# Kernel optimization log

Measured on AMD Instinct MI355X. Metric: run time of the kernel, lower is better.

Reference implementation:

```python
import jax, jax.numpy as jnp
import numpy as np

B, F, CTX, HID, L, NB = 16384, 64, 128, 512, 8, 2


def setup_inputs() -> dict:
    key = jax.random.key(0)
    ks = jax.random.split(key, 8)
    inputs = jax.random.normal(ks[0], (B, F), jnp.float32)
    context = jax.random.normal(ks[1], (B, CTX), jnp.float32)
    n_id = F // 2                      # identity features per coupling layer
    in_dim = n_id + CTX                # coupling net input = identity half + context
    out_dim = F                        # 2 * num_transform_features (shift | scale)
    s_in = 1.0 / np.sqrt(in_dim)
    s_h = 1.0 / np.sqrt(HID)
    W_in = jax.random.uniform(ks[2], (L, in_dim, HID), jnp.float32, -s_in, s_in)
    b_in = jax.random.uniform(ks[3], (L, HID), jnp.float32, -s_in, s_in)
    W_h = jax.random.uniform(ks[4], (L, NB, HID, HID), jnp.float32, -s_h, s_h)
    b_h = jax.random.uniform(ks[5], (L, NB, HID), jnp.float32, -s_h, s_h)
    # output layer init: normal(0, 0.01) weight, zero bias (as in torch source)
    W_out = 0.01 * jax.random.normal(ks[6], (L, HID, out_dim), jnp.float32)
    b_out = jnp.zeros((L, out_dim), jnp.float32)
    # fixed random permutations between coupling layers (nflows RandomPermutation buffers)
    rng = np.random.RandomState(42)
    perms = jnp.asarray(np.stack([rng.permutation(F) for _ in range(L - 1)]), jnp.int32)
    return dict(inputs=inputs, context=context, W_in=W_in, b_in=b_in,
                W_h=W_h, b_h=b_h, W_out=W_out, b_out=b_out, perms=perms)


def reference(inputs, context, W_in, b_in, W_h, b_h, W_out, b_out, perms):
    F_ = inputs.shape[-1]
    n_layers = W_in.shape[0]
    n_blocks = W_h.shape[1]
    nt = F_ // 2  # num transform features
    even_idx = jnp.arange(0, F_, 2)
    odd_idx = jnp.arange(1, F_, 2)
    x = jnp.clip(inputs, -1.0, 1.0)
    logdet = jnp.zeros(x.shape[0], x.dtype)
    for i in range(n_layers):
        # mask[::2]=1 for even layers -> mask>0 (even indices) are TRANSFORM features
        if i % 2 == 0:
            t_idx, id_idx = even_idx, odd_idx
        else:
            t_idx, id_idx = odd_idx, even_idx
        id_split = x[:, id_idx]   # [B, nt]
        tr_split = x[:, t_idx]    # [B, nt]
        h = jax.nn.relu(jnp.concatenate([id_split, context], -1) @ W_in[i] + b_in[i])
        for j in range(n_blocks):
            h = jax.nn.relu(h @ W_h[i, j] + b_h[i, j])
        p = h @ W_out[i] + b_out[i]            # [B, 2*nt]
        shift = p[:, :nt]
        scale = jax.nn.sigmoid(p[:, nt:] + 2.0) + 1e-3
        logdet = logdet + jnp.sum(jnp.log(scale), axis=-1)
        x = x.at[:, t_idx].set(tr_split * scale + shift).at[:, id_idx].set(id_split)
        if i < n_layers - 1:
            x = x[:, perms[i]]
    return jnp.clip(x, -1.0, 1.0), logdet
```

## Files before the change

kernel.cpp:

```cpp
#include <hip/hip_runtime.h>


typedef float v4f  __attribute__((ext_vector_type(4)));
typedef float v16f __attribute__((ext_vector_type(16)));
typedef int   v4i  __attribute__((ext_vector_type(4)));
typedef int   v8i  __attribute__((ext_vector_type(8)));
typedef unsigned char uchar;
typedef unsigned long long ull;

#define BATCH 16384
#define NF    64
#define NCTX  128
#define NL    8

#define RS     528
#define HHALF  256
#define AST    208
#define AHALF  96
#define PST    68

#define WSCALE     16.0f
#define WSCALE_INV 0.0625f

#define WIN_EPL   (192 * 512)
#define WH_EPB    (512 * 512)
#define WOUT_EPL  (512 * 64)
#define OFF_WIN   ((size_t)0)
#define OFF_WH    ((size_t)(8 * WIN_EPL))
#define OFF_WOUT  (OFF_WH + (size_t)(16 * WH_EPB))
#define TOT_PACK_ELEMS (OFF_WOUT + (size_t)(8 * WOUT_EPL))
#define NEED_WS   (TOT_PACK_ELEMS)

template<bool HI>
__device__ __forceinline__ unsigned int pk2(float a, float b, unsigned int old) {
    return __builtin_amdgcn_cvt_pk_fp8_f32(a, b, old, HI);
}
__device__ __forceinline__ uchar q8(float v) {
    return (uchar)(__builtin_amdgcn_cvt_pk_fp8_f32(v, v, 0u, false) & 0xffu);
}

__global__ void pack_weights_kernel(const float* __restrict__ W_in,
                                    const float* __restrict__ W_h,
                                    const float* __restrict__ W_out,
                                    unsigned char* __restrict__ ws) {
    const int TIN  = 8 * (WIN_EPL / 8);
    const int TH   = 16 * (WH_EPB / 8);
    const int TOUT = 8 * (WOUT_EPL / 8);
    int t = blockIdx.x * blockDim.x + threadIdx.x;
    if (t >= TIN + TH + TOUT) return;
    float v[8];
    if (t < TIN + TH) {
        const float* src; int r, rawK;
        if (t < TIN) {
            int i = t / (WIN_EPL / 8); r = t - i * (WIN_EPL / 8);
            src = W_in + (size_t)i * (160 * 512); rawK = 160;
        } else {
            int u = t - TIN; int ij = u >> 15; r = u & 32767;
            src = W_h + (size_t)ij * WH_EPB; rawK = 512;
        }
        int kb  = r >> 12, rem = r & 4095;
        int ls  = rem >> 2, g = rem & 3;
        int lane = ls & 63;
        int n = (ls >> 6) * 32 + (lane & 31);
        int pig = (g == 1) ? 2 : (g == 2) ? 1 : g;
        int k0 = kb * 64 + (lane >> 5) * 32 + pig * 8;
#pragma unroll
        for (int j = 0; j < 8; ++j) {
            int k = k0 + j;
            v[j] = (k < rawK) ? src[(size_t)k * 512 + n] * WSCALE : 0.f;
        }
    } else {
        int u = t - TIN - TH;
        int i = u >> 12, r = u & 4095;
        const float* src = W_out + (size_t)i * WOUT_EPL;
        int frag = r >> 6, lane = r & 63;
        int k0 = (frag >> 2) * 32 + (lane >> 4) * 8;
        int n  = (frag & 3) * 16 + (lane & 15);
#pragma unroll
        for (int j = 0; j < 8; ++j)
            v[j] = src[(size_t)(k0 + j) * 64 + n] * WSCALE;
    }
    uint2 o;
    o.x = pk2<false>(v[0], v[1], 0u);
    o.x = pk2<true >(v[2], v[3], o.x);
    o.y = pk2<false>(v[4], v[5], 0u);
    o.y = pk2<true >(v[6], v[7], o.y);
    *(uint2*)(ws + (size_t)t * 8) = o;
}

__device__ __forceinline__ v16f mfma32(ull a, ull b, v16f c) {
    return __builtin_amdgcn_mfma_f32_32x32x16_fp8_fp8((long)a, (long)b, c, 0, 0, 0);
}
__device__ __forceinline__ v4f mfma16(ull a, ull b, v4f c) {
    return __builtin_amdgcn_mfma_f32_16x16x32_fp8_fp8((long)a, (long)b, c, 0, 0, 0);
}
__device__ __forceinline__ v16f mfma64(v8i a, v8i b, v16f c) {
    return __builtin_amdgcn_mfma_scale_f32_32x32x64_f8f6f4(
        a, b, c, 0, 0, 0, 0x7f7f7f7f, 0, 0x7f7f7f7f);
}

template<int NKB>
__device__ __forceinline__ void gemm32mx(
    const uchar* __restrict__ wpk,
    const float* __restrict__ bias,
    const uchar* __restrict__ Abuf, int ast, int halfoff,
    uchar* __restrict__ Obuf,
    int strip, int lane)
{
    const int l31 = lane & 31, hl = lane >> 5;
    v16f acc0, acc1;
#pragma unroll
    for (int r = 0; r < 16; ++r) { acc0[r] = 0.f; acc1[r] = 0.f; }
    const uchar* aLo0 = Abuf + l31 * ast + hl * 16;
    const uchar* aHi0 = aLo0 + halfoff;
    const uchar* aLo1 = aLo0 + 32 * ast;
    const uchar* aHi1 = aHi0 + 32 * ast;
    const uchar* bptr = wpk + (size_t)(strip * 64 + lane) * 32;

    auto loadB = [&](int kb) -> v8i {
        if (kb >= NKB) kb = NKB - 1;
        const uchar* p = bptr + (size_t)kb * 32768;
        v4i lo = *(const v4i*)p;
        v4i hi = *(const v4i*)(p + 16);
        return __builtin_shufflevector(lo, hi, 0, 1, 2, 3, 4, 5, 6, 7);
    };
    auto loadA = [&](const uchar* lo_, const uchar* hi_, int kb) -> v8i {
        v4i lo = *(const v4i*)(lo_ + kb * 32);
        v4i hi = *(const v4i*)(hi_ + kb * 32);
        return __builtin_shufflevector(lo, hi, 0, 1, 2, 3, 4, 5, 6, 7);
    };

    v8i b0 = loadB(0), b1 = loadB(1), b2 = loadB(2), b3 = loadB(3);
#pragma unroll 1
    for (int kb = 0; kb + 3 < NKB; kb += 4) {
        acc0 = mfma64(loadA(aLo0, aHi0, kb + 0), b0, acc0);
        acc1 = mfma64(loadA(aLo1, aHi1, kb + 0), b0, acc1);
        b0 = loadB(kb + 4);
        acc0 = mfma64(loadA(aLo0, aHi0, kb + 1), b1, acc0);
        acc1 = mfma64(loadA(aLo1, aHi1, kb + 1), b1, acc1);
        b1 = loadB(kb + 5);
        acc0 = mfma64(loadA(aLo0, aHi0, kb + 2), b2, acc0);
        acc1 = mfma64(loadA(aLo1, aHi1, kb + 2), b2, acc1);
        b2 = loadB(kb + 6);
        acc0 = mfma64(loadA(aLo0, aHi0, kb + 3), b3, acc0);
        acc1 = mfma64(loadA(aLo1, aHi1, kb + 3), b3, acc1);
        b3 = loadB(kb + 7);
    }
    if constexpr ((NKB & 3) != 0) {
        constexpr int kb0 = NKB & ~3;
#pragma unroll
        for (int kb = kb0; kb < NKB; ++kb) {
            v8i bb = ((kb & 3) == 0) ? b0 : ((kb & 3) == 1) ? b1
                   : ((kb & 3) == 2) ? b2 : b3;
            acc0 = mfma64(loadA(aLo0, aHi0, kb), bb, acc0);
            acc1 = mfma64(loadA(aLo1, aHi1, kb), bb, acc1);
        }
    }

    const int n = strip * 32 + l31;
    const int nb = ((n >> 3) & 1) * HHALF + ((n >> 4) << 3) + (n & 7);
    const float bv = bias[n];
#pragma unroll
    for (int reg = 0; reg < 16; ++reg) {
        int row = (reg & 3) + 8 * (reg >> 2) + 4 * hl;
        float v0 = fmaxf(fmaf(acc0[reg], WSCALE_INV, bv), 0.f);
        Obuf[row * RS + nb] = q8(v0);
        float v1 = fmaxf(fmaf(acc1[reg], WSCALE_INV, bv), 0.f);
        Obuf[(row + 32) * RS + nb] = q8(v1);
    }
}

template<int KC>
__device__ __forceinline__ void gemm32_raw(
    const float* __restrict__ wraw,
    const float* __restrict__ bias,
    const uchar* __restrict__ Abuf, int ast, int ahalf,
    uchar* __restrict__ Obuf,
    int strip, int lane)
{
    constexpr int P = KC / 2;
    const int l31 = lane & 31, hl = lane >> 5;
    v16f acc0, acc1;
#pragma unroll
    for (int r = 0; r < 16; ++r) { acc0[r] = 0.f; acc1[r] = 0.f; }
    const uchar* a0p = Abuf + l31 * ast + hl * ahalf;
    const uchar* a1p = a0p + 32 * ast;

    auto loadB = [&](int kc) -> ull {
        if (kc >= KC) kc = KC - 1;
        int n  = strip * 32 + l31;
        int k0 = kc * 16 + hl * 8;
        unsigned int lo, hi;
        lo = pk2<false>(wraw[(size_t)(k0 + 0) * 512 + n] * WSCALE,
                        wraw[(size_t)(k0 + 1) * 512 + n] * WSCALE, 0u);
        lo = pk2<true >(wraw[(size_t)(k0 + 2) * 512 + n] * WSCALE,
                        wraw[(size_t)(k0 + 3) * 512 + n] * WSCALE, lo);
        hi = pk2<false>(wraw[(size_t)(k0 + 4) * 512 + n] * WSCALE,
                        wraw[(size_t)(k0 + 5) * 512 + n] * WSCALE, 0u);
        hi = pk2<true >(wraw[(size_t)(k0 + 6) * 512 + n] * WSCALE,
                        wraw[(size_t)(k0 + 7) * 512 + n] * WSCALE, hi);
        return ((ull)hi << 32) | (ull)lo;
    };

    ull b0 = loadB(0), b1 = loadB(1), b2 = loadB(2), b3 = loadB(3);
    int p2 = 0;
#pragma unroll 1
    for (; p2 + 1 < P; p2 += 2) {
        ulonglong2 Aa0 = *(const ulonglong2*)(a0p + p2 * 16);
        ulonglong2 Aa1 = *(const ulonglong2*)(a1p + p2 * 16);
        acc0 = mfma32(Aa0.x, b0, acc0);
        acc1 = mfma32(Aa1.x, b0, acc1);
        b0 = loadB(2 * p2 + 4);
        acc0 = mfma32(Aa0.y, b1, acc0);
        acc1 = mfma32(Aa1.y, b1, acc1);
        b1 = loadB(2 * p2 + 5);
        ulonglong2 Ab0 = *(const ulonglong2*)(a0p + p2 * 16 + 16);
        ulonglong2 Ab1 = *(const ulonglong2*)(a1p + p2 * 16 + 16);
        acc0 = mfma32(Ab0.x, b2, acc0);
        acc1 = mfma32(Ab1.x, b2, acc1);
        b2 = loadB(2 * p2 + 6);
        acc0 = mfma32(Ab0.y, b3, acc0);
        acc1 = mfma32(Ab1.y, b3, acc1);
        b3 = loadB(2 * p2 + 7);
    }
    if constexpr (P & 1) {
        ulonglong2 Aa0 = *(const ulonglong2*)(a0p + (P - 1) * 16);
        ulonglong2 Aa1 = *(const ulonglong2*)(a1p + (P - 1) * 16);
        acc0 = mfma32(Aa0.x, b0, acc0);
        acc1 = mfma32(Aa1.x, b0, acc1);
        acc0 = mfma32(Aa0.y, b1, acc0);
        acc1 = mfma32(Aa1.y, b1, acc1);
    }

    const int n = strip * 32 + l31;
    const int nb = ((n >> 3) & 1) * HHALF + ((n >> 4) << 3) + (n & 7);
    const float bv = bias[n];
#pragma unroll
    for (int reg = 0; reg < 16; ++reg) {
        int row = (reg & 3) + 8 * (reg >> 2) + 4 * hl;
        float v0 = fmaxf(fmaf(acc0[reg], WSCALE_INV, bv), 0.f);
        Obuf[row * RS + nb] = q8(v0);
        float v1 = fmaxf(fmaf(acc1[reg], WSCALE_INV, bv), 0.f);
        Obuf[(row + 32) * RS + nb] = q8(v1);
    }
}

template<bool PACKED>
__device__ __forceinline__ void gemm16_out(
    const uchar* __restrict__ wpk,
    const float* __restrict__ wraw,
    const float* __restrict__ bias,
    const uchar* __restrict__ Abuf,
    float* __restrict__ Pbuf,
    int mtb, int ntb, int lane)
{
    const int quad = lane >> 4, l15 = lane & 15;
    v4f acc; acc[0] = acc[1] = acc[2] = acc[3] = 0.f;
    const int row = mtb * 16 + l15;
    const uchar* ap = Abuf + row * RS + (quad & 1) * HHALF + ((quad >> 1) << 3);
    const uchar* bptr =
        PACKED ? wpk + (size_t)(ntb * 64 + lane) * 8 : (const uchar*)0;
    constexpr int KC = 16;

    auto loadB = [&](int kc) -> ull {
        if (kc >= KC) kc = KC - 1;
        if constexpr (PACKED) {
            return *(const ull*)(bptr + (size_t)kc * 2048);
        } else {
            int n  = ntb * 16 + l15;
            int k0 = kc * 32 + quad * 8;
            unsigned int lo, hi;
            lo = pk2<false>(wraw[(size_t)(k0 + 0) * 64 + n] * WSCALE,
                            wraw[(size_t)(k0 + 1) * 64 + n] * WSCALE, 0u);
            lo = pk2<true >(wraw[(size_t)(k0 + 2) * 64 + n] * WSCALE,
                            wraw[(size_t)(k0 + 3) * 64 + n] * WSCALE, lo);
            hi = pk2<false>(wraw[(size_t)(k0 + 4) * 64 + n] * WSCALE,
                            wraw[(size_t)(k0 + 5) * 64 + n] * WSCALE, 0u);
            hi = pk2<true >(wraw[(size_t)(k0 + 6) * 64 + n] * WSCALE,
                            wraw[(size_t)(k0 + 7) * 64 + n] * WSCALE, hi);
            return ((ull)hi << 32) | (ull)lo;
        }
    };
    auto step = [&](int kc, ull bb) {
        ull a = *(const ull*)(ap + kc * 16);
        acc = mfma16(a, bb, acc);
    };

    ull b0 = loadB(0), b1 = loadB(1), b2 = loadB(2), b3 = loadB(3);
    int kc = 0;
#pragma unroll 1
    for (; kc + 3 < KC; kc += 4) {
        step(kc + 0, b0); b0 = loadB(kc + 4);
        step(kc + 1, b1); b1 = loadB(kc + 5);
        step(kc + 2, b2); b2 = loadB(kc + 6);
        step(kc + 3, b3); b3 = loadB(kc + 7);
    }

    const int n = ntb * 16 + l15;
    const float bv = bias[n];
#pragma unroll
    for (int r = 0; r < 4; ++r)
        Pbuf[(mtb * 16 + quad * 4 + r) * PST + n] = fmaf(acc[r], WSCALE_INV, bv);
}

template<bool PACKED>
__global__ __launch_bounds__(1024, 4) void flow_kernel(
    const float* __restrict__ inputs,
    const float* __restrict__ ctx,
    const float* __restrict__ W_in,  const float* __restrict__ b_in,
    const float* __restrict__ W_h,   const float* __restrict__ b_h,
    const float* __restrict__ W_out, const float* __restrict__ b_out,
    const int*   __restrict__ perms,
    const uchar* __restrict__ wpk,
    float* __restrict__ out)
{
    __shared__ __align__(16) uchar hbuf0[64 * RS];
    __shared__ __align__(16) uchar hbuf1[64 * RS];
    __shared__ __align__(16) uchar abuf[64 * AST];
    __shared__ __align__(16) float xbuf[64 * NF];
    __shared__ int permsh[NF];

    float* pbuf    = (float*)hbuf1;
    float* scratch = (float*)hbuf0;

    const int tid  = threadIdx.x;
    const int wave = tid >> 6;
    const int lane = tid & 63;
    const int trow = tid >> 4;
    const int tq   = tid & 15;
    const int row0 = blockIdx.x * 64;

    {
        float4 v = ((const float4*)(inputs + (size_t)row0 * NF))[tid];
        v.x = fminf(fmaxf(v.x, -1.f), 1.f);
        v.y = fminf(fmaxf(v.y, -1.f), 1.f);
        v.z = fminf(fmaxf(v.z, -1.f), 1.f);
        v.w = fminf(fmaxf(v.w, -1.f), 1.f);
        ((float4*)xbuf)[tid] = v;
    }
    {
        const float* crow = ctx + (size_t)(row0 + trow) * NCTX + tq * 8;
        float4 f0 = ((const float4*)crow)[0];
        float4 f1 = ((const float4*)crow)[1];
        uint2 ck;
        ck.x = pk2<false>(f0.x, f0.y, 0u);
        ck.x = pk2<true >(f0.z, f0.w, ck.x);
        ck.y = pk2<false>(f1.x, f1.y, 0u);
        ck.y = pk2<true >(f1.z, f1.w, ck.y);
        *(uint2*)(abuf + trow * AST + (tq & 1) * AHALF + (2 + (tq >> 1)) * 8) = ck;
    }
    if (tid < 256) {
        int r = tid >> 2, q = tid & 3;
        *(ull*)(abuf + r * AST + (q & 1) * AHALF + 80 + ((q >> 1) << 3)) = 0ULL;
    }
    float ld_acc = 0.f;
    __syncthreads();

#pragma unroll 1
    for (int i = 0; i < NL; ++i) {
        const int par = i & 1;
        const int idp = par ^ 1;

        if (tq < 4) {
            const float* xr = xbuf + trow * NF + idp;
            uint2 idv;
            idv.x = pk2<false>(xr[2 * (tq * 8 + 0)], xr[2 * (tq * 8 + 1)], 0u);
            idv.x = pk2<true >(xr[2 * (tq * 8 + 2)], xr[2 * (tq * 8 + 3)], idv.x);
            idv.y = pk2<false>(xr[2 * (tq * 8 + 4)], xr[2 * (tq * 8 + 5)], 0u);
            idv.y = pk2<true >(xr[2 * (tq * 8 + 6)], xr[2 * (tq * 8 + 7)], idv.y);
            *(uint2*)(abuf + trow * AST + (tq & 1) * AHALF + ((tq >> 1) << 3)) = idv;
        }
        __syncthreads();

        if constexpr (PACKED) {
            gemm32mx<3>(wpk + OFF_WIN + (size_t)i * WIN_EPL, b_in + i * 512,
                        abuf, AST, AHALF, hbuf0, wave, lane);
            __syncthreads();
            gemm32mx<8>(wpk + OFF_WH + (size_t)(i * 2 + 0) * WH_EPB,
                        b_h + (i * 2 + 0) * 512,
                        hbuf0, RS, HHALF, hbuf1, wave, lane);
            __syncthreads();
            gemm32mx<8>(wpk + OFF_WH + (size_t)(i * 2 + 1) * WH_EPB,
                        b_h + (i * 2 + 1) * 512,
                        hbuf1, RS, HHALF, hbuf0, wave, lane);
            __syncthreads();
        } else {
            gemm32_raw<10>(W_in + (size_t)i * (160 * 512), b_in + i * 512,
                           abuf, AST, AHALF, hbuf0, wave, lane);
            __syncthreads();
            gemm32_raw<32>(W_h + (size_t)(i * 2 + 0) * WH_EPB,
                           b_h + (i * 2 + 0) * 512,
                           hbuf0, RS, HHALF, hbuf1, wave, lane);
            __syncthreads();
            gemm32_raw<32>(W_h + (size_t)(i * 2 + 1) * WH_EPB,
                           b_h + (i * 2 + 1) * 512,
                           hbuf1, RS, HHALF, hbuf0, wave, lane);
            __syncthreads();
        }
        gemm16_out<PACKED>(
            PACKED ? wpk + OFF_WOUT + (size_t)i * WOUT_EPL : (const uchar*)0,
            W_out + (size_t)i * WOUT_EPL, b_out + i * 64,
            hbuf0, pbuf, wave >> 2, wave & 3, lane);
        __syncthreads();

        {
#pragma unroll
            for (int j = 0; j < 2; ++j) {
                int sc = tq * 2 + j;
                float shiftv = pbuf[trow * PST + sc];
                float z = pbuf[trow * PST + 32 + sc] + 2.0f;
                float s = 1.0f / (1.0f + __expf(-z)) + 0.001f;
                int tc = 2 * sc + par;
                xbuf[trow * NF + tc] = xbuf[trow * NF + tc] * s + shiftv;
                ld_acc += __logf(s);
            }
        }
        __syncthreads();

        if (i < NL - 1) {
            ((float4*)scratch)[tid] = ((float4*)xbuf)[tid];
            if (tid < NF) permsh[tid] = perms[i * NF + tid];
            __syncthreads();
#pragma unroll
            for (int j = 0; j < 4; ++j) {
                int c = tq * 4 + j;
                xbuf[trow * NF + c] = scratch[trow * NF + permsh[c]];
            }
            __syncthreads();
        }
    }

    {
        float4 v = ((float4*)xbuf)[tid];
        v.x = fminf(fmaxf(v.x, -1.f), 1.f);
        v.y = fminf(fmaxf(v.y, -1.f), 1.f);
        v.z = fminf(fmaxf(v.z, -1.f), 1.f);
        v.w = fminf(fmaxf(v.w, -1.f), 1.f);
        ((float4*)(out + (size_t)row0 * NF))[tid] = v;
    }
    ld_acc += __shfl_down(ld_acc, 1);
    ld_acc += __shfl_down(ld_acc, 2);
    ld_acc += __shfl_down(ld_acc, 4);
    ld_acc += __shfl_down(ld_acc, 8);
    if (tq == 0) out[(size_t)BATCH * NF + row0 + trow] = ld_acc;
}

extern "C" void kernel_launch(void* const* d_in, const int* in_sizes, int n_in,
                              void* d_out, int out_size, void* d_ws, size_t ws_size,
                              hipStream_t stream) {
    const float* inputs  = (const float*)d_in[0];
    const float* context = (const float*)d_in[1];
    const float* W_in    = (const float*)d_in[2];
    const float* b_in    = (const float*)d_in[3];
    const float* W_h     = (const float*)d_in[4];
    const float* b_h     = (const float*)d_in[5];
    const float* W_out   = (const float*)d_in[6];
    const float* b_out   = (const float*)d_in[7];
    const int*   perms   = (const int*)d_in[8];
    float* out = (float*)d_out;

    if (ws_size >= (size_t)NEED_WS) {
        uchar* ws = (uchar*)d_ws;
        const int total_threads = (int)(TOT_PACK_ELEMS / 8);
        pack_weights_kernel<<<(total_threads + 255) / 256, 256, 0, stream>>>(
            W_in, W_h, W_out, ws);
        flow_kernel<true><<<256, 1024, 0, stream>>>(
            inputs, context, W_in, b_in, W_h, b_h, W_out, b_out, perms, ws, out);
    } else {
        flow_kernel<false><<<256, 1024, 0, stream>>>(
            inputs, context, W_in, b_in, W_h, b_h, W_out, b_out, perms,
            (const uchar*)0, out);
    }
}
```

Measured before the change: 213.5 us.

## Halve block to 512 threads with 2x2 MFMA register tiling per wave

Drops the block from 1024 to 512 threads. Each wave now computes two 32-column strips of the hidden GEMMs, keeping four accumulators so every A fragment loaded from LDS feeds two B fragments, with operand order swapped so outputs pack into 4-byte LDS stores. The output GEMM does two row tiles per wave and writes float4 results, and elementwise loops are widened to match. The aim is more reuse of A and B per load and fewer LDS write instructions, at the cost of more accumulator registers and fewer waves to hide latency.

```diff
diff --git a/kernel.cpp b/kernel.cpp
--- a/kernel.cpp
+++ b/kernel.cpp
@@ -105,21 +105,22 @@
     const float* __restrict__ bias,
     const uchar* __restrict__ Abuf, int ast, int halfoff,
     uchar* __restrict__ Obuf,
-    int strip, int lane)
+    int pair, int lane)
 {
     const int l31 = lane & 31, hl = lane >> 5;
-    v16f acc0, acc1;
-#pragma unroll
-    for (int r = 0; r < 16; ++r) { acc0[r] = 0.f; acc1[r] = 0.f; }
+    v16f a00, a01, a10, a11;
+#pragma unroll
+    for (int r = 0; r < 16; ++r) { a00[r] = 0.f; a01[r] = 0.f;
+                                   a10[r] = 0.f; a11[r] = 0.f; }
     const uchar* aLo0 = Abuf + l31 * ast + hl * 16;
     const uchar* aHi0 = aLo0 + halfoff;
     const uchar* aLo1 = aLo0 + 32 * ast;
     const uchar* aHi1 = aHi0 + 32 * ast;
-    const uchar* bptr = wpk + (size_t)(strip * 64 + lane) * 32;
-
-    auto loadB = [&](int kb) -> v8i {
+    const uchar* bp = wpk + (size_t)(pair * 128 + lane) * 32;
+
+    auto loadB = [&](int s, int kb) -> v8i {
         if (kb >= NKB) kb = NKB - 1;
-        const uchar* p = bptr + (size_t)kb * 32768;
+        const uchar* p = bp + s * 2048 + (size_t)kb * 32768;
         v4i lo = *(const v4i*)p;
         v4i hi = *(const v4i*)(p + 16);
         return __builtin_shufflevector(lo, hi, 0, 1, 2, 3, 4, 5, 6, 7);
@@ -130,44 +131,59 @@
         return __builtin_shufflevector(lo, hi, 0, 1, 2, 3, 4, 5, 6, 7);
     };
 
-    v8i b0 = loadB(0), b1 = loadB(1), b2 = loadB(2), b3 = loadB(3);
+    v8i b00 = loadB(0, 0), b10 = loadB(1, 0);
+    v8i b01 = loadB(0, 1), b11 = loadB(1, 1);
+    int kb = 0;
 #pragma unroll 1
-    for (int kb = 0; kb + 3 < NKB; kb += 4) {
-        acc0 = mfma64(loadA(aLo0, aHi0, kb + 0), b0, acc0);
-        acc1 = mfma64(loadA(aLo1, aHi1, kb + 0), b0, acc1);
-        b0 = loadB(kb + 4);
-        acc0 = mfma64(loadA(aLo0, aHi0, kb + 1), b1, acc0);
-        acc1 = mfma64(loadA(aLo1, aHi1, kb + 1), b1, acc1);
-        b1 = loadB(kb + 5);
-        acc0 = mfma64(loadA(aLo0, aHi0, kb + 2), b2, acc0);
-        acc1 = mfma64(loadA(aLo1, aHi1, kb + 2), b2, acc1);
-        b2 = loadB(kb + 6);
-        acc0 = mfma64(loadA(aLo0, aHi0, kb + 3), b3, acc0);
-        acc1 = mfma64(loadA(aLo1, aHi1, kb + 3), b3, acc1);
-        b3 = loadB(kb + 7);
-    }
-    if constexpr ((NKB & 3) != 0) {
-        constexpr int kb0 = NKB & ~3;
-#pragma unroll
-        for (int kb = kb0; kb < NKB; ++kb) {
-            v8i bb = ((kb & 3) == 0) ? b0 : ((kb & 3) == 1) ? b1
-                   : ((kb & 3) == 2) ? b2 : b3;
-            acc0 = mfma64(loadA(aLo0, aHi0, kb), bb, acc0);
-            acc1 = mfma64(loadA(aLo1, aHi1, kb), bb, acc1);
-        }
-    }
-
-    const int n = strip * 32 + l31;
-    const int nb = ((n >> 3) & 1) * HHALF + ((n >> 4) << 3) + (n & 7);
-    const float bv = bias[n];
-#pragma unroll
-    for (int reg = 0; reg < 16; ++reg) {
-        int row = (reg & 3) + 8 * (reg >> 2) + 4 * hl;
-        float v0 = fmaxf(fmaf(acc0[reg], WSCALE_INV, bv), 0.f);
-        Obuf[row * RS + nb] = q8(v0);
-        float v1 = fmaxf(fmaf(acc1[reg], WSCALE_INV, bv), 0.f);
-        Obuf[(row + 32) * RS + nb] = q8(v1);
-    }
+    for (; kb + 1 < NKB; kb += 2) {
+        v8i x0 = loadA(aLo0, aHi0, kb);
+        v8i x1 = loadA(aLo1, aHi1, kb);
+        a00 = mfma64(b00, x0, a00);
+        a01 = mfma64(b00, x1, a01);
+        a10 = mfma64(b10, x0, a10);
+        a11 = mfma64(b10, x1, a11);
+        b00 = loadB(0, kb + 2); b10 = loadB(1, kb + 2);
+        x0 = loadA(aLo0, aHi0, kb + 1);
+        x1 = loadA(aLo1, aHi1, kb + 1);
+        a00 = mfma64(b01, x0, a00);
+        a01 = mfma64(b01, x1, a01);
+        a10 = mfma64(b11, x0, a10);
+        a11 = mfma64(b11, x1, a11);
+        b01 = loadB(0, kb + 3); b11 = loadB(1, kb + 3);
+    }
+    if constexpr (NKB & 1) {
+        v8i x0 = loadA(aLo0, aHi0, NKB - 1);
+        v8i x1 = loadA(aLo1, aHi1, NKB - 1);
+        a00 = mfma64(b00, x0, a00);
+        a01 = mfma64(b00, x1, a01);
+        a10 = mfma64(b10, x0, a10);
+        a11 = mfma64(b10, x1, a11);
+    }
+
+    const uchar* ob0 = Obuf + l31 * RS + 4 * hl;
+    const uchar* ob1 = ob0 + 32 * RS;
+    auto emit = [&](const v16f& am0, const v16f& am1, int strip) {
+#pragma unroll
+        for (int q = 0; q < 4; ++q) {
+            const int n0 = strip * 32 + q * 8 + 4 * hl;
+            float4 bv = *(const float4*)(bias + n0);
+            unsigned int u0, u1;
+            u0 = pk2<false>(fmaxf(fmaf(am0[4 * q + 0], WSCALE_INV, bv.x), 0.f),
+                            fmaxf(fmaf(am0[4 * q + 1], WSCALE_INV, bv.y), 0.f), 0u);
+            u0 = pk2<true >(fmaxf(fmaf(am0[4 * q + 2], WSCALE_INV, bv.z), 0.f),
+                            fmaxf(fmaf(am0[4 * q + 3], WSCALE_INV, bv.w), 0.f), u0);
+            u1 = pk2<false>(fmaxf(fmaf(am1[4 * q + 0], WSCALE_INV, bv.x), 0.f),
+                            fmaxf(fmaf(am1[4 * q + 1], WSCALE_INV, bv.y), 0.f), 0u);
+            u1 = pk2<true >(fmaxf(fmaf(am1[4 * q + 2], WSCALE_INV, bv.z), 0.f),
+                            fmaxf(fmaf(am1[4 * q + 3], WSCALE_INV, bv.w), 0.f), u1);
+            const int g = strip * 4 + q;
+            const int off = (g & 1) * HHALF + ((g >> 1) << 3);
+            *(unsigned int*)(ob0 + off) = u0;
+            *(unsigned int*)(ob1 + off) = u1;
+        }
+    };
+    emit(a00, a01, pair * 2 + 0);
+    emit(a10, a11, pair * 2 + 1);
 }
 
 template<int KC>
@@ -252,12 +268,18 @@
     const float* __restrict__ bias,
     const uchar* __restrict__ Abuf,
     float* __restrict__ Pbuf,
-    int mtb, int ntb, int lane)
+    int w, int lane)
 {
     const int quad = lane >> 4, l15 = lane & 15;
-    v4f acc; acc[0] = acc[1] = acc[2] = acc[3] = 0.f;
-    const int row = mtb * 16 + l15;
-    const uchar* ap = Abuf + row * RS + (quad & 1) * HHALF + ((quad >> 1) << 3);
+    const int ntb  = w & 3;
+    const int mtb0 = w >> 2;
+    const int row0 = mtb0 * 16 + l15;
+    const int row1 = row0 + 32;
+    v4f acc0, acc1;
+    acc0[0] = acc0[1] = acc0[2] = acc0[3] = 0.f;
+    acc1[0] = acc1[1] = acc1[2] = acc1[3] = 0.f;
+    const uchar* ap0 = Abuf + row0 * RS + (quad & 1) * HHALF + ((quad >> 1) << 3);
+    const uchar* ap1 = Abuf + row1 * RS + (quad & 1) * HHALF + ((quad >> 1) << 3);
     const uchar* bptr =
         PACKED ? wpk + (size_t)(ntb * 64 + lane) * 8 : (const uchar*)0;
     constexpr int KC = 16;
@@ -282,8 +304,10 @@
         }
     };
     auto step = [&](int kc, ull bb) {
-        ull a = *(const ull*)(ap + kc * 16);
-        acc = mfma16(a, bb, acc);
+        ull a0 = *(const ull*)(ap0 + kc * 16);
+        acc0 = mfma16(bb, a0, acc0);
+        ull a1 = *(const ull*)(ap1 + kc * 16);
+        acc1 = mfma16(bb, a1, acc1);
     };
 
     ull b0 = loadB(0), b1 = loadB(1), b2 = loadB(2), b3 = loadB(3);
@@ -296,15 +320,22 @@
         step(kc + 3, b3); b3 = loadB(kc + 7);
     }
 
-    const int n = ntb * 16 + l15;
-    const float bv = bias[n];
-#pragma unroll
-    for (int r = 0; r < 4; ++r)
-        Pbuf[(mtb * 16 + quad * 4 + r) * PST + n] = fmaf(acc[r], WSCALE_INV, bv);
+    float4 bv = *(const float4*)(bias + ntb * 16 + quad * 4);
+    float4 o0, o1;
+    o0.x = fmaf(acc0[0], WSCALE_INV, bv.x);
+    o0.y = fmaf(acc0[1], WSCALE_INV, bv.y);
+    o0.z = fmaf(acc0[2], WSCALE_INV, bv.z);
+    o0.w = fmaf(acc0[3], WSCALE_INV, bv.w);
+    *(float4*)(Pbuf + row0 * PST + ntb * 16 + quad * 4) = o0;
+    o1.x = fmaf(acc1[0], WSCALE_INV, bv.x);
+    o1.y = fmaf(acc1[1], WSCALE_INV, bv.y);
+    o1.z = fmaf(acc1[2], WSCALE_INV, bv.z);
+    o1.w = fmaf(acc1[3], WSCALE_INV, bv.w);
+    *(float4*)(Pbuf + row1 * PST + ntb * 16 + quad * 4) = o1;
 }
 
 template<bool PACKED>
-__global__ __launch_bounds__(1024, 4) void flow_kernel(
+__global__ __launch_bounds__(512, 2) void flow_kernel(
     const float* __restrict__ inputs,
     const float* __restrict__ ctx,
     const float* __restrict__ W_in,  const float* __restrict__ b_in,
@@ -326,28 +357,38 @@
     const int tid  = threadIdx.x;
     const int wave = tid >> 6;
     const int lane = tid & 63;
-    const int trow = tid >> 4;
-    const int tq   = tid & 15;
+    const int trow = tid >> 3;
+    const int t8   = tid & 7;
     const int row0 = blockIdx.x * 64;
 
     {
-        float4 v = ((const float4*)(inputs + (size_t)row0 * NF))[tid];
-        v.x = fminf(fmaxf(v.x, -1.f), 1.f);
-        v.y = fminf(fmaxf(v.y, -1.f), 1.f);
-        v.z = fminf(fmaxf(v.z, -1.f), 1.f);
-        v.w = fminf(fmaxf(v.w, -1.f), 1.f);
-        ((float4*)xbuf)[tid] = v;
+#pragma unroll
+        for (int j = 0; j < 2; ++j) {
+            float4 v = ((const float4*)(inputs + (size_t)row0 * NF))[tid + j * 512];
+            v.x = fminf(fmaxf(v.x, -1.f), 1.f);
+            v.y = fminf(fmaxf(v.y, -1.f), 1.f);
+            v.z = fminf(fmaxf(v.z, -1.f), 1.f);
+            v.w = fminf(fmaxf(v.w, -1.f), 1.f);
+            ((float4*)xbuf)[tid + j * 512] = v;
+        }
     }
     {
-        const float* crow = ctx + (size_t)(row0 + trow) * NCTX + tq * 8;
+        const float* crow = ctx + (size_t)(row0 + trow) * NCTX + t8 * 16;
         float4 f0 = ((const float4*)crow)[0];
         float4 f1 = ((const float4*)crow)[1];
-        uint2 ck;
-        ck.x = pk2<false>(f0.x, f0.y, 0u);
-        ck.x = pk2<true >(f0.z, f0.w, ck.x);
-        ck.y = pk2<false>(f1.x, f1.y, 0u);
-        ck.y = pk2<true >(f1.z, f1.w, ck.y);
-        *(uint2*)(abuf + trow * AST + (tq & 1) * AHALF + (2 + (tq >> 1)) * 8) = ck;
+        float4 f2 = ((const float4*)crow)[2];
+        float4 f3 = ((const float4*)crow)[3];
+        uint2 ck0, ck1;
+        ck0.x = pk2<false>(f0.x, f0.y, 0u);
+        ck0.x = pk2<true >(f0.z, f0.w, ck0.x);
+        ck0.y = pk2<false>(f1.x, f1.y, 0u);
+        ck0.y = pk2<true >(f1.z, f1.w, ck0.y);
+        ck1.x = pk2<false>(f2.x, f2.y, 0u);
+        ck1.x = pk2<true >(f2.z, f2.w, ck1.x);
+        ck1.y = pk2<false>(f3.x, f3.y, 0u);
+        ck1.y = pk2<true >(f3.z, f3.w, ck1.y);
+        *(uint2*)(abuf + trow * AST + (2 + t8) * 8) = ck0;
+        *(uint2*)(abuf + trow * AST + AHALF + (2 + t8) * 8) = ck1;
     }
     if (tid < 256) {
         int r = tid >> 2, q = tid & 3;
@@ -361,14 +402,14 @@
         const int par = i & 1;
         const int idp = par ^ 1;
 
-        if (tq < 4) {
+        if (t8 < 4) {
             const float* xr = xbuf + trow * NF + idp;
             uint2 idv;
-            idv.x = pk2<false>(xr[2 * (tq * 8 + 0)], xr[2 * (tq * 8 + 1)], 0u);
-            idv.x = pk2<true >(xr[2 * (tq * 8 + 2)], xr[2 * (tq * 8 + 3)], idv.x);
-            idv.y = pk2<false>(xr[2 * (tq * 8 + 4)], xr[2 * (tq * 8 + 5)], 0u);
-            idv.y = pk2<true >(xr[2 * (tq * 8 + 6)], xr[2 * (tq * 8 + 7)], idv.y);
-            *(uint2*)(abuf + trow * AST + (tq & 1) * AHALF + ((tq >> 1) << 3)) = idv;
+            idv.x = pk2<false>(xr[2 * (t8 * 8 + 0)], xr[2 * (t8 * 8 + 1)], 0u);
+            idv.x = pk2<true >(xr[2 * (t8 * 8 + 2)], xr[2 * (t8 * 8 + 3)], idv.x);
+            idv.y = pk2<false>(xr[2 * (t8 * 8 + 4)], xr[2 * (t8 * 8 + 5)], 0u);
+            idv.y = pk2<true >(xr[2 * (t8 * 8 + 6)], xr[2 * (t8 * 8 + 7)], idv.y);
+            *(uint2*)(abuf + trow * AST + (t8 & 1) * AHALF + ((t8 >> 1) << 3)) = idv;
         }
         __syncthreads();
 
@@ -386,27 +427,35 @@
             __syncthreads();
         } else {
             gemm32_raw<10>(W_in + (size_t)i * (160 * 512), b_in + i * 512,
-                           abuf, AST, AHALF, hbuf0, wave, lane);
+                           abuf, AST, AHALF, hbuf0, wave * 2 + 0, lane);
+            gemm32_raw<10>(W_in + (size_t)i * (160 * 512), b_in + i * 512,
+                           abuf, AST, AHALF, hbuf0, wave * 2 + 1, lane);
             __syncthreads();
             gemm32_raw<32>(W_h + (size_t)(i * 2 + 0) * WH_EPB,
                            b_h + (i * 2 + 0) * 512,
-                           hbuf0, RS, HHALF, hbuf1, wave, lane);
+                           hbuf0, RS, HHALF, hbuf1, wave * 2 + 0, lane);
+            gemm32_raw<32>(W_h + (size_t)(i * 2 + 0) * WH_EPB,
+                           b_h + (i * 2 + 0) * 512,
+                           hbuf0, RS, HHALF, hbuf1, wave * 2 + 1, lane);
             __syncthreads();
             gemm32_raw<32>(W_h + (size_t)(i * 2 + 1) * WH_EPB,
                            b_h + (i * 2 + 1) * 512,
-                           hbuf1, RS, HHALF, hbuf0, wave, lane);
+                           hbuf1, RS, HHALF, hbuf0, wave * 2 + 0, lane);
+            gemm32_raw<32>(W_h + (size_t)(i * 2 + 1) * WH_EPB,
+                           b_h + (i * 2 + 1) * 512,
+                           hbuf1, RS, HHALF, hbuf0, wave * 2 + 1, lane);
             __syncthreads();
         }
         gemm16_out<PACKED>(
             PACKED ? wpk + OFF_WOUT + (size_t)i * WOUT_EPL : (const uchar*)0,
             W_out + (size_t)i * WOUT_EPL, b_out + i * 64,
-            hbuf0, pbuf, wave >> 2, wave & 3, lane);
+            hbuf0, pbuf, wave, lane);
         __syncthreads();
 
         {
 #pragma unroll
-            for (int j = 0; j < 2; ++j) {
-                int sc = tq * 2 + j;
+            for (int j = 0; j < 4; ++j) {
+                int sc = t8 * 4 + j;
                 float shiftv = pbuf[trow * PST + sc];
                 float z = pbuf[trow * PST + 32 + sc] + 2.0f;
                 float s = 1.0f / (1.0f + __expf(-z)) + 0.001f;
@@ -418,12 +467,13 @@
         __syncthreads();
 
         if (i < NL - 1) {
-            ((float4*)scratch)[tid] = ((float4*)xbuf)[tid];
+            ((float4*)scratch)[tid]       = ((float4*)xbuf)[tid];
+            ((float4*)scratch)[tid + 512] = ((float4*)xbuf)[tid + 512];
             if (tid < NF) permsh[tid] = perms[i * NF + tid];
             __syncthreads();
 #pragma unroll
-            for (int j = 0; j < 4; ++j) {
-                int c = tq * 4 + j;
+            for (int j = 0; j < 8; ++j) {
+                int c = t8 * 8 + j;
                 xbuf[trow * NF + c] = scratch[trow * NF + permsh[c]];
             }
             __syncthreads();
@@ -431,18 +481,20 @@
     }
 
     {
-        float4 v = ((float4*)xbuf)[tid];
-        v.x = fminf(fmaxf(v.x, -1.f), 1.f);
-        v.y = fminf(fmaxf(v.y, -1.f), 1.f);
-        v.z = fminf(fmaxf(v.z, -1.f), 1.f);
-        v.w = fminf(fmaxf(v.w, -1.f), 1.f);
-        ((float4*)(out + (size_t)row0 * NF))[tid] = v;
+#pragma unroll
+        for (int j = 0; j < 2; ++j) {
+            float4 v = ((float4*)xbuf)[tid + j * 512];
+            v.x = fminf(fmaxf(v.x, -1.f), 1.f);
+            v.y = fminf(fmaxf(v.y, -1.f), 1.f);
+            v.z = fminf(fmaxf(v.z, -1.f), 1.f);
+            v.w = fminf(fmaxf(v.w, -1.f), 1.f);
+            ((float4*)(out + (size_t)row0 * NF))[tid + j * 512] = v;
+        }
     }
     ld_acc += __shfl_down(ld_acc, 1);
     ld_acc += __shfl_down(ld_acc, 2);
     ld_acc += __shfl_down(ld_acc, 4);
-    ld_acc += __shfl_down(ld_acc, 8);
-    if (tq == 0) out[(size_t)BATCH * NF + row0 + trow] = ld_acc;
+    if (t8 == 0) out[(size_t)BATCH * NF + row0 + trow] = ld_acc;
 }
 
 extern "C" void kernel_launch(void* const* d_in, const int* in_sizes, int n_in,
@@ -464,10 +516,10 @@
         const int total_threads = (int)(TOT_PACK_ELEMS / 8);
         pack_weights_kernel<<<(total_threads + 255) / 256, 256, 0, stream>>>(
             W_in, W_h, W_out, ws);
-        flow_kernel<true><<<256, 1024, 0, stream>>>(
+        flow_kernel<true><<<256, 512, 0, stream>>>(
             inputs, context, W_in, b_in, W_h, b_h, W_out, b_out, perms, ws, out);
     } else {
-        flow_kernel<false><<<256, 1024, 0, stream>>>(
+        flow_kernel<false><<<256, 512, 0, stream>>>(
             inputs, context, W_in, b_in, W_h, b_h, W_out, b_out, perms,
             (const uchar*)0, out);
     }
```

New measurement: 200.3 us. -6.2%, faster.
